# Kernel tuning notes

Measured on AMD Instinct MI355X. Metric: run time of the kernel, lower is better.

## Reference

```python
import jax, jax.numpy as jnp
import numpy as np

D_MODEL = 1024
NHEAD = 16
HEAD_DIM = D_MODEL // NHEAD
DFF = 4096
EPS = 1e-5


def _layernorm(x, g, b):
    mu = jnp.mean(x, axis=-1, keepdims=True)
    var = jnp.mean(jnp.square(x - mu), axis=-1, keepdims=True)
    return (x - mu) * jax.lax.rsqrt(var + EPS) * g + b


def setup_inputs() -> dict:
    key = jax.random.key(0)
    ks = jax.random.split(key, 20)
    B, S = 2, 2048
    s = 0.02
    inp = {
        "src": jax.random.normal(ks[0], (B, S, D_MODEL), jnp.float32),
        "recompute_idx": jnp.sort(jax.random.randint(ks[1], (409,), 0, S)),
        "cached_k": jax.random.normal(ks[2], (B, NHEAD, S, HEAD_DIM), jnp.float32),
        "cached_v": jax.random.normal(ks[3], (B, NHEAD, S, HEAD_DIM), jnp.float32),
        "Wq": jax.random.normal(ks[4], (D_MODEL, D_MODEL), jnp.float32) * s,
        "bq": jnp.zeros((D_MODEL,), jnp.float32),
        "Wk": jax.random.normal(ks[5], (D_MODEL, D_MODEL), jnp.float32) * s,
        "bk": jnp.zeros((D_MODEL,), jnp.float32),
        "Wv": jax.random.normal(ks[6], (D_MODEL, D_MODEL), jnp.float32) * s,
        "bv": jnp.zeros((D_MODEL,), jnp.float32),
        "Wo": jax.random.normal(ks[7], (D_MODEL, D_MODEL), jnp.float32) * s,
        "bo": jnp.zeros((D_MODEL,), jnp.float32),
        "W1": jax.random.normal(ks[8], (DFF, D_MODEL), jnp.float32) * s,
        "b1": jnp.zeros((DFF,), jnp.float32),
        "W2": jax.random.normal(ks[9], (D_MODEL, DFF), jnp.float32) * s,
        "b2": jnp.zeros((D_MODEL,), jnp.float32),
        "g1": jnp.ones((D_MODEL,), jnp.float32),
        "beta1": jnp.zeros((D_MODEL,), jnp.float32),
        "g2": jnp.ones((D_MODEL,), jnp.float32),
        "beta2": jnp.zeros((D_MODEL,), jnp.float32),
    }
    return inp


def reference(src, recompute_idx, cached_k, cached_v, Wq, bq, Wk, bk, Wv, bv,
              Wo, bo, W1, b1, W2, b2, g1, beta1, g2, beta2):
    B, S, D = src.shape
    H, hd = NHEAD, HEAD_DIM

    # Q for all tokens
    q = (src @ Wq.T + bq).reshape(B, S, H, hd).transpose(0, 2, 1, 3)  # [B,H,S,hd]

    # K/V recomputed only for selected tokens, scattered over cached KV
    src_rec = src[:, recompute_idx, :]  # [B,R,D]
    R = src_rec.shape[1]
    k_rec = (src_rec @ Wk.T + bk).reshape(B, R, H, hd).transpose(0, 2, 1, 3)
    v_rec = (src_rec @ Wv.T + bv).reshape(B, R, H, hd).transpose(0, 2, 1, 3)
    k_full = cached_k.at[:, :, recompute_idx, :].set(k_rec)  # [B,H,S,hd]
    v_full = cached_v.at[:, :, recompute_idx, :].set(v_rec)

    # attention over mixed cached/fresh KV
    scores = jnp.einsum('bhqd,bhkd->bhqk', q, k_full) / np.sqrt(hd).astype(src.dtype)
    probs = jax.nn.softmax(scores, axis=-1)
    attn = jnp.einsum('bhqk,bhkd->bhqd', probs, v_full)
    attn = attn.transpose(0, 2, 1, 3).reshape(B, S, D)
    attn = attn @ Wo.T + bo

    x = _layernorm(src + attn, g1, beta1)
    ff = jax.nn.relu(x @ W1.T + b1) @ W2.T + b2
    x = _layernorm(x + ff, g2, beta2)
    return x
```

## Files before the change

### kernel.cpp

```cpp
#include <hip/hip_runtime.h>
#include <hip/hip_bf16.h>

typedef __attribute__((ext_vector_type(4))) float f32x4;
typedef __attribute__((ext_vector_type(8))) short s16x8;
typedef __attribute__((ext_vector_type(4))) short s16x4;
typedef __attribute__((ext_vector_type(2))) short s16x2;

typedef __attribute__((address_space(1))) const unsigned int guint;
typedef __attribute__((address_space(3))) unsigned int luint;

#define D_MODEL 1024
#define NHEAD 16
#define HEAD_DIM 64
#define DFF 4096
#define SEQ 2048
#define BATCH 2

__device__ __forceinline__ float b2f(short s) {
  union { unsigned int u; float f; } v;
  v.u = ((unsigned int)(unsigned short)s) << 16;
  return v.f;
}
__device__ __forceinline__ short f2b(float f) {
  __hip_bfloat16 h = __float2bfloat16(f);
  return *reinterpret_cast<short*>(&h);
}
__device__ __forceinline__ s16x8 cvt8(f32x4 a, f32x4 b) {
  s16x8 r;
  #pragma unroll
  for (int i = 0; i < 4; ++i) { r[i] = f2b(a[i]); r[i + 4] = f2b(b[i]); }
  return r;
}

template<int MODE, bool AF32, bool WF32>
__global__ __launch_bounds__(256, 3)
void gemm_nt(const void* __restrict__ Av, const void* __restrict__ Wv,
             const float* __restrict__ bias, short* __restrict__ out,
             int M, int N, int K,
             const int* __restrict__ idx, int R,
             const float* __restrict__ bias2)
{
  constexpr bool GLDS = (!AF32 && !WF32);

  const float* Af = (const float*)Av;
  const short* Ab = (const short*)Av;
  const float* Wf = (const float*)Wv;
  const short* Wb = (const short*)Wv;

  const int tid  = threadIdx.x;
  const int lane = tid & 63, wave = tid >> 6;
  const int g = lane >> 4, l15 = lane & 15;
  const int wm = (wave & 1) * 64, wn = (wave >> 1) * 64;

  const int z = (MODE == 6 || MODE == 7) ? blockIdx.z : 0;

  const int nwg = gridDim.x * gridDim.y;
  int lid = blockIdx.y * gridDim.x + blockIdx.x;
  if ((nwg & 7) == 0) lid = (lid & 7) * (nwg >> 3) + (lid >> 3);
  const int bn = lid % gridDim.x, bm = lid / gridDim.x;

  f32x4 acc[4][4] = {};

  if constexpr (GLDS) {
    __shared__ short As[2][128][32];
    __shared__ short Bs[2][128][32];

    const short* Wbase = Wb + ((MODE == 7) ? ((size_t)z << 20) : 0);
    const int kOff = (MODE == 6) ? z * 2048 : 0;
    const int Keff = (MODE == 6) ? 2048 : K;

    const int rA0 = wave * 16 + (lane >> 2);
    const int rA1 = rA0 + 64;
    const int c0  = (lane & 3) * 8;

    auto arow = [&](int r) -> long {
      const int gm = bm * 128 + r;
      const int am = gm < M ? gm : M - 1;
      if (MODE == 3 || MODE == 4 || MODE == 7) {
        const int b0 = am / R;
        return (long)(b0 * SEQ + idx[am - b0 * R]);
      }
      return am;
    };
    const long aR0 = arow(rA0), aR1 = arow(rA1);
    const long wR0 = bn * 128 + rA0, wR1 = bn * 128 + rA1;

    const short* gA0 = Ab + aR0 * K + kOff + c0;
    const short* gA1 = Ab + aR1 * K + kOff + c0;
    const short* gB0 = Wbase + wR0 * K + kOff + c0;
    const short* gB1 = Wbase + wR1 * K + kOff + c0;

    auto stage = [&](int buf, int k0) {
      luint* lA0 = (luint*)((short*)As + buf * 4096 + wave * 512);
      luint* lA1 = (luint*)((short*)As + buf * 4096 + (4 + wave) * 512);
      luint* lB0 = (luint*)((short*)Bs + buf * 4096 + wave * 512);
      luint* lB1 = (luint*)((short*)Bs + buf * 4096 + (4 + wave) * 512);
      __builtin_amdgcn_global_load_lds((guint*)(gA0 + k0), lA0, 16, 0, 0);
      __builtin_amdgcn_global_load_lds((guint*)(gA1 + k0), lA1, 16, 0, 0);
      __builtin_amdgcn_global_load_lds((guint*)(gB0 + k0), lB0, 16, 0, 0);
      __builtin_amdgcn_global_load_lds((guint*)(gB1 + k0), lB1, 16, 0, 0);
    };

    stage(0, 0);
    __syncthreads();
    int cur = 0;
    for (int k0 = 0; k0 < Keff; k0 += 32) {
      const int k1 = k0 + 32;
      if (k1 < Keff) stage(cur ^ 1, k1);

      s16x8 af[4], bf4[4];
      #pragma unroll
      for (int mi = 0; mi < 4; ++mi)
        af[mi] = *(const s16x8*)&As[cur][wm + mi * 16 + l15][g * 8];
      #pragma unroll
      for (int ni = 0; ni < 4; ++ni)
        bf4[ni] = *(const s16x8*)&Bs[cur][wn + ni * 16 + l15][g * 8];
      #pragma unroll
      for (int mi = 0; mi < 4; ++mi)
        #pragma unroll
        for (int ni = 0; ni < 4; ++ni)
          acc[mi][ni] = __builtin_amdgcn_mfma_f32_16x16x32_bf16(af[mi], bf4[ni], acc[mi][ni], 0, 0, 0);

      __syncthreads();
      cur ^= 1;
    }
  } else {
    __shared__ short As[128][40];
    __shared__ short Bs[128][40];
    const int r0 = tid >> 1, c0 = (tid & 1) * 16;
    const int gm0 = bm * 128 + r0;
    const int am0 = gm0 < M ? gm0 : M - 1;
    long aRow0;
    if (MODE == 3 || MODE == 4) {
      const int b0 = am0 / R;
      aRow0 = (long)(b0 * SEQ + idx[am0 - b0 * R]);
    } else {
      aRow0 = am0;
    }
    const long wRow0 = bn * 128 + r0;

    for (int k0 = 0; k0 < K; k0 += 32) {
      __syncthreads();
      if (AF32) {
        f32x4 a0 = *(const f32x4*)(Af + aRow0 * K + k0 + c0);
        f32x4 a1 = *(const f32x4*)(Af + aRow0 * K + k0 + c0 + 4);
        f32x4 a2 = *(const f32x4*)(Af + aRow0 * K + k0 + c0 + 8);
        f32x4 a3 = *(const f32x4*)(Af + aRow0 * K + k0 + c0 + 12);
        *(s16x8*)&As[r0][c0]     = cvt8(a0, a1);
        *(s16x8*)&As[r0][c0 + 8] = cvt8(a2, a3);
      } else {
        *(s16x8*)&As[r0][c0]     = *(const s16x8*)(Ab + aRow0 * K + k0 + c0);
        *(s16x8*)&As[r0][c0 + 8] = *(const s16x8*)(Ab + aRow0 * K + k0 + c0 + 8);
      }
      if (WF32) {
        f32x4 w0 = *(const f32x4*)(Wf + wRow0 * K + k0 + c0);
        f32x4 w1 = *(const f32x4*)(Wf + wRow0 * K + k0 + c0 + 4);
        f32x4 w2 = *(const f32x4*)(Wf + wRow0 * K + k0 + c0 + 8);
        f32x4 w3 = *(const f32x4*)(Wf + wRow0 * K + k0 + c0 + 12);
        *(s16x8*)&Bs[r0][c0]     = cvt8(w0, w1);
        *(s16x8*)&Bs[r0][c0 + 8] = cvt8(w2, w3);
      } else {
        *(s16x8*)&Bs[r0][c0]     = *(const s16x8*)(Wb + wRow0 * K + k0 + c0);
        *(s16x8*)&Bs[r0][c0 + 8] = *(const s16x8*)(Wb + wRow0 * K + k0 + c0 + 8);
      }
      __syncthreads();

      s16x8 af[4], bf4[4];
      #pragma unroll
      for (int mi = 0; mi < 4; ++mi)
        af[mi] = *(const s16x8*)&As[wm + mi * 16 + l15][g * 8];
      #pragma unroll
      for (int ni = 0; ni < 4; ++ni)
        bf4[ni] = *(const s16x8*)&Bs[wn + ni * 16 + l15][g * 8];
      #pragma unroll
      for (int mi = 0; mi < 4; ++mi)
        #pragma unroll
        for (int ni = 0; ni < 4; ++ni)
          acc[mi][ni] = __builtin_amdgcn_mfma_f32_16x16x32_bf16(af[mi], bf4[ni], acc[mi][ni], 0, 0, 0);
    }
  }

  #pragma unroll
  for (int mi = 0; mi < 4; ++mi) {
    #pragma unroll
    for (int ni = 0; ni < 4; ++ni) {
      const int gn = bn * 128 + wn + ni * 16 + l15;
      float bv;
      if (MODE == 6)      bv = 0.f;
      else if (MODE == 7) bv = z ? bias2[gn] : bias[gn];
      else                bv = bias[gn];
      #pragma unroll
      for (int r = 0; r < 4; ++r) {
        const int gm = bm * 128 + wm + mi * 16 + g * 4 + r;
        if (gm >= M) continue;
        float v = acc[mi][ni][r] + bv;
        if (MODE == 1) v = v > 0.f ? v : 0.f;
        if (MODE == 2) v *= 0.125f;
        if (MODE == 0 || MODE == 1) {
          out[(long)gm * N + gn] = f2b(v);
        } else if (MODE == 2) {
          const int b = gm >> 11, s = gm & (SEQ - 1);
          const int h = gn >> 6, d = gn & 63;
          out[(((long)(b * NHEAD + h)) * SEQ + s) * 64 + d] = f2b(v);
        } else if (MODE == 3) {
          const int b = gm / R, s = idx[gm - b * R];
          const int h = gn >> 6, d = gn & 63;
          out[(((long)(b * NHEAD + h)) * SEQ + s) * 64 + d] = f2b(v);
        } else if (MODE == 4) {
          const int b = gm / R, s = idx[gm - b * R];
          const int h = gn >> 6, d = gn & 63;
          out[(((long)(b * NHEAD + h)) * 64 + d) * SEQ + s] = f2b(v);
        } else if (MODE == 6) {
          out[((long)z << 22) + (long)gm * N + gn] = f2b(v);
        } else {
          const int b = gm / R, s = idx[gm - b * R];
          const int h = gn >> 6, d = gn & 63;
          if (z == 0)
            out[(((long)(b * NHEAD + h)) * SEQ + s) * 64 + d] = f2b(v);
          else
            (out + (1L << 22))[(((long)(b * NHEAD + h)) * 64 + d) * SEQ + s] = f2b(v);
        }
      }
    }
  }
}

__global__ __launch_bounds__(256, 2)
void attn_fwd(const short* __restrict__ Q, const short* __restrict__ Kf,
              const short* __restrict__ Vt, short* __restrict__ out)
{
  __shared__ short Kl[2][64][64];
  __shared__ short Vl[2][64][64];

  const int tid  = threadIdx.x;
  const int lane = tid & 63, w = tid >> 6;
  const int g = lane >> 4, l15 = lane & 15;
  const int bh = blockIdx.x;
  const int qt = blockIdx.y;
  const int b  = bh >> 4, h = bh & 15;

  const long base = (long)bh * SEQ * 64;
  const int  q0   = qt * 128 + w * 32;

  s16x8 qf[2][2];
  #pragma unroll
  for (int mi = 0; mi < 2; ++mi)
    #pragma unroll
    for (int c = 0; c < 2; ++c)
      qf[mi][c] = *(const s16x8*)(Q + base + (long)(q0 + mi * 16 + l15) * 64 + c * 32 + g * 8);

  float lsum[2] = {0.f, 0.f};
  f32x4 o[2][4] = {};

  auto ldsw = [](short (*buf)[64], int row, int slot) -> short* {
    return (short*)((char*)&buf[0][0] + row * 128 + ((slot ^ (row & 7)) << 4));
  };

  const int c20 = tid, c21 = tid + 256;
  const int r0 = c20 >> 3, s0 = c20 & 7;
  const int r1 = c21 >> 3, s1 = c21 & 7;

  s16x8 kr[2], vr[2];
  kr[0] = *(const s16x8*)(Kf + base + (long)r0 * 64 + s0 * 8);
  kr[1] = *(const s16x8*)(Kf + base + (long)r1 * 64 + s1 * 8);
  vr[0] = *(const s16x8*)(Vt + base + (long)r0 * SEQ + s0 * 8);
  vr[1] = *(const s16x8*)(Vt + base + (long)r1 * SEQ + s1 * 8);
  *(s16x8*)ldsw(Kl[0], r0, s0) = kr[0];
  *(s16x8*)ldsw(Kl[0], r1, s1) = kr[1];
  *(s16x8*)ldsw(Vl[0], r0, s0) = vr[0];
  *(s16x8*)ldsw(Vl[0], r1, s1) = vr[1];

  int cur = 0;
  for (int t = 0; t < SEQ / 64; ++t) {
    __syncthreads();
    const int kvn = (t + 1) * 64;
    if (kvn < SEQ) {
      kr[0] = *(const s16x8*)(Kf + base + (long)(kvn + r0) * 64 + s0 * 8);
      kr[1] = *(const s16x8*)(Kf + base + (long)(kvn + r1) * 64 + s1 * 8);
      vr[0] = *(const s16x8*)(Vt + base + (long)r0 * SEQ + kvn + s0 * 8);
      vr[1] = *(const s16x8*)(Vt + base + (long)r1 * SEQ + kvn + s1 * 8);
    }

    f32x4 sc[2][4] = {};
    __builtin_amdgcn_s_setprio(1);
    #pragma unroll
    for (int c = 0; c < 2; ++c)
      #pragma unroll
      for (int n = 0; n < 4; ++n) {
        s16x8 kb = *(const s16x8*)ldsw(Kl[cur], n * 16 + l15, c * 4 + g);
        sc[0][n] = __builtin_amdgcn_mfma_f32_16x16x32_bf16(kb, qf[0][c], sc[0][n], 0, 0, 0);
        sc[1][n] = __builtin_amdgcn_mfma_f32_16x16x32_bf16(kb, qf[1][c], sc[1][n], 0, 0, 0);
      }
    __builtin_amdgcn_s_setprio(0);

    s16x8 pa[2][2];
    #pragma unroll
    for (int mi = 0; mi < 2; ++mi) {
      #pragma unroll
      for (int n = 0; n < 4; ++n)
        #pragma unroll
        for (int r = 0; r < 4; ++r) {
          sc[mi][n][r] = __expf(sc[mi][n][r]);
          lsum[mi] += sc[mi][n][r];
        }
      unsigned int wpk[4][2];
      #pragma unroll
      for (int n = 0; n < 4; ++n)
        #pragma unroll
        for (int p = 0; p < 2; ++p)
          asm("v_cvt_pk_bf16_f32 %0, %1, %2"
              : "=v"(wpk[n][p]) : "v"(sc[mi][n][2 * p]), "v"(sc[mi][n][2 * p + 1]));
      #pragma unroll
      for (int c = 0; c < 2; ++c) {
        union { s16x8 v; unsigned int u[4]; } pu;
        #pragma unroll
        for (int p = 0; p < 2; ++p) {
          unsigned int a = wpk[2 * c][p], bb = wpk[2 * c + 1][p];
          asm volatile("v_permlane32_swap_b32 %0, %1" : "+v"(a), "+v"(bb));
          asm volatile("v_permlane16_swap_b32 %0, %1" : "+v"(a), "+v"(bb));
          pu.u[p]     = a;
          pu.u[2 + p] = bb;
        }
        pa[mi][c] = pu.v;
      }
    }

    __builtin_amdgcn_s_setprio(1);
    #pragma unroll
    for (int dt = 0; dt < 4; ++dt)
      #pragma unroll
      for (int c = 0; c < 2; ++c) {
        s16x8 vb = *(const s16x8*)ldsw(Vl[cur], dt * 16 + l15, c * 4 + g);
        o[0][dt] = __builtin_amdgcn_mfma_f32_16x16x32_bf16(pa[0][c], vb, o[0][dt], 0, 0, 0);
        o[1][dt] = __builtin_amdgcn_mfma_f32_16x16x32_bf16(pa[1][c], vb, o[1][dt], 0, 0, 0);
      }
    __builtin_amdgcn_s_setprio(0);

    if (kvn < SEQ) {
      *(s16x8*)ldsw(Kl[cur ^ 1], r0, s0) = kr[0];
      *(s16x8*)ldsw(Kl[cur ^ 1], r1, s1) = kr[1];
      *(s16x8*)ldsw(Vl[cur ^ 1], r0, s0) = vr[0];
      *(s16x8*)ldsw(Vl[cur ^ 1], r1, s1) = vr[1];
    }
    cur ^= 1;
  }

  float inv[2][4];
  #pragma unroll
  for (int mi = 0; mi < 2; ++mi) {
    float tt = lsum[mi];
    tt += __shfl_xor(tt, 16, 64);
    tt += __shfl_xor(tt, 32, 64);
    #pragma unroll
    for (int r = 0; r < 4; ++r)
      inv[mi][r] = 1.0f / __shfl(tt, g * 4 + r, 64);
  }

  #pragma unroll
  for (int mi = 0; mi < 2; ++mi)
    #pragma unroll
    for (int dt = 0; dt < 4; ++dt)
      #pragma unroll
      for (int r = 0; r < 4; ++r) {
        const int q   = q0 + mi * 16 + g * 4 + r;
        const int col = h * 64 + dt * 16 + l15;
        out[((long)(b * SEQ + q)) * D_MODEL + col] = f2b(o[mi][dt][r] * inv[mi][r]);
      }
}

template<bool RES_F32, bool OUT_F32>
__global__ __launch_bounds__(256, 4)
void ln_res(const short* __restrict__ a, const void* __restrict__ resv,
            const float* __restrict__ g, const float* __restrict__ beta,
            void* __restrict__ outv)
{
  __shared__ float red[8];
  const int row = blockIdx.x;
  const int tid = threadIdx.x;
  const int lane = tid & 63, w = tid >> 6;

  s16x4 va = *(const s16x4*)(a + (long)row * D_MODEL + tid * 4);
  float x[4];
  if (RES_F32) {
    f32x4 vr = *(const f32x4*)((const float*)resv + (long)row * D_MODEL + tid * 4);
    #pragma unroll
    for (int i = 0; i < 4; ++i) x[i] = b2f(va[i]) + vr[i];
  } else {
    s16x4 vr = *(const s16x4*)((const short*)resv + (long)row * D_MODEL + tid * 4);
    #pragma unroll
    for (int i = 0; i < 4; ++i) x[i] = b2f(va[i]) + b2f(vr[i]);
  }
  float sum = x[0] + x[1] + x[2] + x[3];
  #pragma unroll
  for (int msk = 32; msk >= 1; msk >>= 1) sum += __shfl_xor(sum, msk, 64);
  if (lane == 0) red[w] = sum;
  __syncthreads();
  sum = red[0] + red[1] + red[2] + red[3];
  const float mu = sum * (1.f / D_MODEL);

  float sq = 0.f;
  #pragma unroll
  for (int i = 0; i < 4; ++i) { float d = x[i] - mu; sq += d * d; }
  #pragma unroll
  for (int msk = 32; msk >= 1; msk >>= 1) sq += __shfl_xor(sq, msk, 64);
  if (lane == 0) red[4 + w] = sq;
  __syncthreads();
  sq = red[4] + red[5] + red[6] + red[7];
  const float rs = rsqrtf(sq * (1.f / D_MODEL) + 1e-5f);

  if (OUT_F32) {
    f32x4 ov;
    #pragma unroll
    for (int i = 0; i < 4; ++i) {
      const int c = tid * 4 + i;
      ov[i] = (x[i] - mu) * rs * g[c] + beta[c];
    }
    *(f32x4*)((float*)outv + (long)row * D_MODEL + tid * 4) = ov;
  } else {
    s16x4 ov;
    #pragma unroll
    for (int i = 0; i < 4; ++i) {
      const int c = tid * 4 + i;
      ov[i] = f2b((x[i] - mu) * rs * g[c] + beta[c]);
    }
    *(s16x4*)((short*)outv + (long)row * D_MODEL + tid * 4) = ov;
  }
}

__global__ __launch_bounds__(256, 4)
void ln_res_ff(const short* __restrict__ p0, const short* __restrict__ p1,
               const float* __restrict__ b2, const short* __restrict__ xres,
               const float* __restrict__ g, const float* __restrict__ beta,
               float* __restrict__ outv)
{
  __shared__ float red[8];
  const int row = blockIdx.x;
  const int tid = threadIdx.x;
  const int lane = tid & 63, w = tid >> 6;

  s16x4 v0 = *(const s16x4*)(p0 + (long)row * D_MODEL + tid * 4);
  s16x4 v1 = *(const s16x4*)(p1 + (long)row * D_MODEL + tid * 4);
  s16x4 vx = *(const s16x4*)(xres + (long)row * D_MODEL + tid * 4);
  f32x4 vb = *(const f32x4*)(b2 + tid * 4);
  float x[4];
  #pragma unroll
  for (int i = 0; i < 4; ++i)
    x[i] = b2f(vx[i]) + b2f(v0[i]) + b2f(v1[i]) + vb[i];

  float sum = x[0] + x[1] + x[2] + x[3];
  #pragma unroll
  for (int msk = 32; msk >= 1; msk >>= 1) sum += __shfl_xor(sum, msk, 64);
  if (lane == 0) red[w] = sum;
  __syncthreads();
  sum = red[0] + red[1] + red[2] + red[3];
  const float mu = sum * (1.f / D_MODEL);

  float sq = 0.f;
  #pragma unroll
  for (int i = 0; i < 4; ++i) { float d = x[i] - mu; sq += d * d; }
  #pragma unroll
  for (int msk = 32; msk >= 1; msk >>= 1) sq += __shfl_xor(sq, msk, 64);
  if (lane == 0) red[4 + w] = sq;
  __syncthreads();
  sq = red[4] + red[5] + red[6] + red[7];
  const float rs = rsqrtf(sq * (1.f / D_MODEL) + 1e-5f);

  f32x4 ov;
  #pragma unroll
  for (int i = 0; i < 4; ++i) {
    const int c = tid * 4 + i;
    ov[i] = (x[i] - mu) * rs * g[c] + beta[c];
  }
  *(f32x4*)(outv + (long)row * D_MODEL + tid * 4) = ov;
}

__global__ void cvt_all(const float* __restrict__ ck, const float* __restrict__ src,
                        const float* __restrict__ Wq, const float* __restrict__ Wk,
                        const float* __restrict__ Wv, const float* __restrict__ Wo,
                        const float* __restrict__ W1, const float* __restrict__ W2,
                        short* __restrict__ k_ws, short* __restrict__ srcb,
                        short* __restrict__ Wqb, short* __restrict__ W1b,
                        short* __restrict__ W2b)
{
  for (int i = blockIdx.x * blockDim.x + threadIdx.x; i < 5242880;
       i += gridDim.x * blockDim.x) {
    const float* s; short* d; int li;
    if      (i < 1048576) { s = ck;  d = k_ws;           li = i; }
    else if (i < 2097152) { s = src; d = srcb;           li = i - 1048576; }
    else if (i < 2359296) { s = Wq;  d = Wqb;            li = i - 2097152; }
    else if (i < 2621440) { s = Wk;  d = Wqb + 1048576;  li = i - 2359296; }
    else if (i < 2883584) { s = Wv;  d = Wqb + 2097152;  li = i - 2621440; }
    else if (i < 3145728) { s = Wo;  d = Wqb + 3145728;  li = i - 2883584; }
    else if (i < 4194304) { s = W1;  d = W1b;            li = i - 3145728; }
    else                  { s = W2;  d = W2b;            li = i - 4194304; }
    f32x4 v = *(const f32x4*)(s + (long)li * 4);
    s16x4 r;
    #pragma unroll
    for (int j = 0; j < 4; ++j) r[j] = f2b(v[j]);
    *(s16x4*)(d + (long)li * 4) = r;
  }
}

__global__ void cvt_v_t(const float* __restrict__ in, short* __restrict__ out)
{
  const int c2 = blockIdx.x * blockDim.x + threadIdx.x;
  const int bh = c2 >> 14;
  const int rem = c2 & 16383;
  const int d = rem & 63;
  const int s0 = (rem >> 6) << 3;
  s16x8 r;
  #pragma unroll
  for (int j = 0; j < 8; ++j)
    r[j] = f2b(in[((long)bh * SEQ + s0 + j) * 64 + d]);
  *(s16x8*)(out + ((long)bh * 64 + d) * SEQ + s0) = r;
}

__global__ void cvt_f32_bf16(const f32x4* __restrict__ in, s16x4* __restrict__ out, int n4)
{
  for (int i = blockIdx.x * blockDim.x + threadIdx.x; i < n4; i += gridDim.x * blockDim.x) {
    f32x4 v = in[i];
    s16x4 r;
    #pragma unroll
    for (int j = 0; j < 4; ++j) r[j] = f2b(v[j]);
    out[i] = r;
  }
}

extern "C" void kernel_launch(void* const* d_in, const int* in_sizes, int n_in,
                              void* d_out, int out_size, void* d_ws, size_t ws_size,
                              hipStream_t stream)
{
  const float* src = (const float*)d_in[0];
  const int*   idx = (const int*)  d_in[1];
  const float* ck  = (const float*)d_in[2];
  const float* cv  = (const float*)d_in[3];
  const float* Wq  = (const float*)d_in[4];
  const float* bq  = (const float*)d_in[5];
  const float* Wk  = (const float*)d_in[6];
  const float* bk  = (const float*)d_in[7];
  const float* Wv  = (const float*)d_in[8];
  const float* bv  = (const float*)d_in[9];
  const float* Wo  = (const float*)d_in[10];
  const float* bo  = (const float*)d_in[11];
  const float* W1  = (const float*)d_in[12];
  const float* b1  = (const float*)d_in[13];
  const float* W2  = (const float*)d_in[14];
  const float* b2  = (const float*)d_in[15];
  const float* g1  = (const float*)d_in[16];
  const float* be1 = (const float*)d_in[17];
  const float* g2  = (const float*)d_in[18];
  const float* be2 = (const float*)d_in[19];
  float* out = (float*)d_out;

  char* ws = (char*)d_ws;
  const size_t SZ = (size_t)4096 * 1024 * 2;
  short* x_ws    = (short*)(ws);
  short* proj_ws = (short*)(ws + SZ);
  short* q_ws    = (short*)(ws + 2 * SZ);
  short* k_ws    = (short*)(ws + 3 * SZ);
  short* v_ws    = (short*)(ws + 4 * SZ);
  short* attn_ws = (short*)(ws + 5 * SZ);
  short* h_ws    = (short*)(ws + 2 * SZ);
  short* ff_ws   = proj_ws;
  short* W1b     = (short*)(ws + 6 * SZ);
  short* W2b     = (short*)(ws + 7 * SZ);
  short* srcb    = (short*)(ws + 8 * SZ);
  short* Wqb     = (short*)(ws + 9 * SZ);
  short* Wkb     = Wqb + 1048576;
  const bool big = ws_size >= 10 * SZ;

  const int M = BATCH * SEQ;
  const int R = 409;
  const int Mr = BATCH * R;
  const int nkv4 = BATCH * NHEAD * SEQ * HEAD_DIM / 4;

  cvt_v_t<<<2048, 256, 0, stream>>>(cv, v_ws);

  if (big) {
    cvt_all<<<2048, 256, 0, stream>>>(ck, src, Wq, Wk, Wv, Wo, W1, W2,
                                      k_ws, srcb, Wqb, W1b, W2b);

    gemm_nt<2, false, false><<<dim3(8, 32), 256, 0, stream>>>(srcb, Wqb, bq, q_ws, M, 1024, 1024, nullptr, 0, nullptr);
    gemm_nt<7, false, false><<<dim3(8, 7, 2), 256, 0, stream>>>(srcb, Wkb, bk, k_ws, Mr, 1024, 1024, idx, R, bv);
    attn_fwd<<<dim3(BATCH * NHEAD, SEQ / 128), 256, 0, stream>>>(q_ws, k_ws, v_ws, attn_ws);
    gemm_nt<0, false, false><<<dim3(8, 32), 256, 0, stream>>>(attn_ws, Wqb + 3145728, bo, proj_ws, M, 1024, 1024, nullptr, 0, nullptr);
    ln_res<true, false><<<4096, 256, 0, stream>>>(proj_ws, src, g1, be1, x_ws);
    gemm_nt<1, false, false><<<dim3(32, 32), 256, 0, stream>>>(x_ws, W1b, b1, h_ws, M, DFF, 1024, nullptr, 0, nullptr);
    gemm_nt<6, false, false><<<dim3(8, 32, 2), 256, 0, stream>>>(h_ws, W2b, nullptr, srcb, M, 1024, 4096, nullptr, 0, nullptr);
    ln_res_ff<<<4096, 256, 0, stream>>>(srcb, Wqb, b2, x_ws, g2, be2, out);
  } else {
    cvt_f32_bf16<<<2048, 256, 0, stream>>>((const f32x4*)ck, (s16x4*)k_ws, nkv4);
    gemm_nt<2, true, true><<<dim3(8, 32), 256, 0, stream>>>(src, Wq, bq, q_ws, M, 1024, 1024, nullptr, 0, nullptr);
    gemm_nt<3, true, true><<<dim3(8, 7), 256, 0, stream>>>(src, Wk, bk, k_ws, Mr, 1024, 1024, idx, R, nullptr);
    gemm_nt<4, true, true><<<dim3(8, 7), 256, 0, stream>>>(src, Wv, bv, v_ws, Mr, 1024, 1024, idx, R, nullptr);
    attn_fwd<<<dim3(BATCH * NHEAD, SEQ / 128), 256, 0, stream>>>(q_ws, k_ws, v_ws, attn_ws);
    gemm_nt<0, false, true><<<dim3(8, 32), 256, 0, stream>>>(attn_ws, Wo, bo, proj_ws, M, 1024, 1024, nullptr, 0, nullptr);
    ln_res<true, false><<<4096, 256, 0, stream>>>(proj_ws, src, g1, be1, x_ws);
    gemm_nt<1, false, true><<<dim3(32, 32), 256, 0, stream>>>(x_ws, W1, b1, h_ws, M, DFF, 1024, nullptr, 0, nullptr);
    gemm_nt<0, false, true><<<dim3(8, 32), 256, 0, stream>>>(h_ws, W2, b2, ff_ws, M, 1024, DFF, nullptr, 0, nullptr);
    ln_res<false, true><<<4096, 256, 0, stream>>>(ff_ws, x_ws, g2, be2, out);
  }
}
```

Baseline: 275.7 us.

## Merge Q/K/V projections into one launch and split-K the out-proj and FFN2 GEMMs

Folds the V-cache transpose into the bulk conversion kernel and merges the Q projection with the gathered K and V projections into a single grid. The attention output projection is split into 2 K-slices and the second FFN GEMM into 4, with the partial sums added inside the layernorm kernels. The aim is to cut launch count, raise parallelism, and fill more CUs on small GEMMs. In exchange the layernorms read more bf16 partial buffers, and the merged conversion kernel does a strided V transpose.

```diff
diff --git a/kernel.cpp b/kernel.cpp
--- a/kernel.cpp
+++ b/kernel.cpp
@@ -38,7 +38,9 @@
              const float* __restrict__ bias, short* __restrict__ out,
              int M, int N, int K,
              const int* __restrict__ idx, int R,
-             const float* __restrict__ bias2)
+             const float* __restrict__ bias2, const float* __restrict__ bias3,
+             short* __restrict__ pB, short* __restrict__ pC,
+             short* __restrict__ pD)
 {
   constexpr bool GLDS = (!AF32 && !WF32);
 
@@ -52,12 +54,18 @@
   const int g = lane >> 4, l15 = lane & 15;
   const int wm = (wave & 1) * 64, wn = (wave >> 1) * 64;
 
-  const int z = (MODE == 6 || MODE == 7) ? blockIdx.z : 0;
-
   const int nwg = gridDim.x * gridDim.y;
   int lid = blockIdx.y * gridDim.x + blockIdx.x;
   if ((nwg & 7) == 0) lid = (lid & 7) * (nwg >> 3) + (lid >> 3);
-  const int bn = lid % gridDim.x, bm = lid / gridDim.x;
+  const int bn = lid % gridDim.x;
+  const int bm0 = lid / gridDim.x;
+
+  int task = 0, bm = bm0, Mt = M;
+  if (MODE == 8) {
+    if (bm0 < 32)      { task = 0; bm = bm0;      Mt = M; }
+    else if (bm0 < 39) { task = 1; bm = bm0 - 32; Mt = BATCH * R; }
+    else               { task = 2; bm = bm0 - 39; Mt = BATCH * R; }
+  }
 
   f32x4 acc[4][4] = {};
 
@@ -65,9 +73,10 @@
     __shared__ short As[2][128][32];
     __shared__ short Bs[2][128][32];
 
-    const short* Wbase = Wb + ((MODE == 7) ? ((size_t)z << 20) : 0);
-    const int kOff = (MODE == 6) ? z * 2048 : 0;
-    const int Keff = (MODE == 6) ? 2048 : K;
+    const short* Wbase = Wb + ((MODE == 8) ? ((size_t)task << 20) : 0);
+    const int nz   = (MODE == 6) ? gridDim.z : 1;
+    const int Keff = K / nz;
+    const int kOff = (MODE == 6) ? (int)blockIdx.z * Keff : 0;
 
     const int rA0 = wave * 16 + (lane >> 2);
     const int rA1 = rA0 + 64;
@@ -75,8 +84,8 @@
 
     auto arow = [&](int r) -> long {
       const int gm = bm * 128 + r;
-      const int am = gm < M ? gm : M - 1;
-      if (MODE == 3 || MODE == 4 || MODE == 7) {
+      const int am = gm < Mt ? gm : Mt - 1;
+      if (MODE == 8 && task > 0) {
         const int b0 = am / R;
         return (long)(b0 * SEQ + idx[am - b0 * R]);
       }
@@ -180,6 +189,12 @@
     }
   }
 
+  short* outz = out;
+  if (MODE == 6) {
+    const int z = blockIdx.z;
+    outz = (z == 0) ? out : (z == 1) ? pB : (z == 2) ? pC : pD;
+  }
+
   #pragma unroll
   for (int mi = 0; mi < 4; ++mi) {
     #pragma unroll
@@ -187,12 +202,13 @@
       const int gn = bn * 128 + wn + ni * 16 + l15;
       float bv;
       if (MODE == 6)      bv = 0.f;
-      else if (MODE == 7) bv = z ? bias2[gn] : bias[gn];
+      else if (MODE == 8) bv = (task == 0) ? bias[gn] : (task == 1) ? bias2[gn] : bias3[gn];
       else                bv = bias[gn];
       #pragma unroll
       for (int r = 0; r < 4; ++r) {
         const int gm = bm * 128 + wm + mi * 16 + g * 4 + r;
-        if (gm >= M) continue;
+        if (MODE == 8) { if (gm >= Mt) continue; }
+        else           { if (gm >= M)  continue; }
         float v = acc[mi][ni][r] + bv;
         if (MODE == 1) v = v > 0.f ? v : 0.f;
         if (MODE == 2) v *= 0.125f;
@@ -211,14 +227,19 @@
           const int h = gn >> 6, d = gn & 63;
           out[(((long)(b * NHEAD + h)) * 64 + d) * SEQ + s] = f2b(v);
         } else if (MODE == 6) {
-          out[((long)z << 22) + (long)gm * N + gn] = f2b(v);
+          outz[(long)gm * N + gn] = f2b(v);
         } else {
-          const int b = gm / R, s = idx[gm - b * R];
           const int h = gn >> 6, d = gn & 63;
-          if (z == 0)
-            out[(((long)(b * NHEAD + h)) * SEQ + s) * 64 + d] = f2b(v);
-          else
-            (out + (1L << 22))[(((long)(b * NHEAD + h)) * 64 + d) * SEQ + s] = f2b(v);
+          if (task == 0) {
+            const int b = gm >> 11, s = gm & (SEQ - 1);
+            out[(((long)(b * NHEAD + h)) * SEQ + s) * 64 + d] = f2b(v * 0.125f);
+          } else if (task == 1) {
+            const int b = gm / R, s = idx[gm - b * R];
+            (out + (1L << 22))[(((long)(b * NHEAD + h)) * SEQ + s) * 64 + d] = f2b(v);
+          } else {
+            const int b = gm / R, s = idx[gm - b * R];
+            (out + (1L << 23))[(((long)(b * NHEAD + h)) * 64 + d) * SEQ + s] = f2b(v);
+          }
         }
       }
     }
@@ -370,7 +391,8 @@
 
 template<bool RES_F32, bool OUT_F32>
 __global__ __launch_bounds__(256, 4)
-void ln_res(const short* __restrict__ a, const void* __restrict__ resv,
+void ln_ff2(const short* __restrict__ p0, const short* __restrict__ p1,
+            const float* __restrict__ bias, const void* __restrict__ resv,
             const float* __restrict__ g, const float* __restrict__ beta,
             void* __restrict__ outv)
 {
@@ -379,17 +401,20 @@
   const int tid = threadIdx.x;
   const int lane = tid & 63, w = tid >> 6;
 
-  s16x4 va = *(const s16x4*)(a + (long)row * D_MODEL + tid * 4);
+  s16x4 v0 = *(const s16x4*)(p0 + (long)row * D_MODEL + tid * 4);
+  s16x4 v1 = *(const s16x4*)(p1 + (long)row * D_MODEL + tid * 4);
+  f32x4 vb = *(const f32x4*)(bias + tid * 4);
   float x[4];
   if (RES_F32) {
     f32x4 vr = *(const f32x4*)((const float*)resv + (long)row * D_MODEL + tid * 4);
     #pragma unroll
-    for (int i = 0; i < 4; ++i) x[i] = b2f(va[i]) + vr[i];
+    for (int i = 0; i < 4; ++i) x[i] = vr[i] + b2f(v0[i]) + b2f(v1[i]) + vb[i];
   } else {
     s16x4 vr = *(const s16x4*)((const short*)resv + (long)row * D_MODEL + tid * 4);
     #pragma unroll
-    for (int i = 0; i < 4; ++i) x[i] = b2f(va[i]) + b2f(vr[i]);
-  }
+    for (int i = 0; i < 4; ++i) x[i] = b2f(vr[i]) + b2f(v0[i]) + b2f(v1[i]) + vb[i];
+  }
+
   float sum = x[0] + x[1] + x[2] + x[3];
   #pragma unroll
   for (int msk = 32; msk >= 1; msk >>= 1) sum += __shfl_xor(sum, msk, 64);
@@ -428,10 +453,11 @@
 }
 
 __global__ __launch_bounds__(256, 4)
-void ln_res_ff(const short* __restrict__ p0, const short* __restrict__ p1,
-               const float* __restrict__ b2, const short* __restrict__ xres,
-               const float* __restrict__ g, const float* __restrict__ beta,
-               float* __restrict__ outv)
+void ln_ff4(const short* __restrict__ p0, const short* __restrict__ p1,
+            const short* __restrict__ p2, const short* __restrict__ p3,
+            const float* __restrict__ bias, const short* __restrict__ xres,
+            const float* __restrict__ g, const float* __restrict__ beta,
+            float* __restrict__ outv)
 {
   __shared__ float red[8];
   const int row = blockIdx.x;
@@ -440,12 +466,14 @@
 
   s16x4 v0 = *(const s16x4*)(p0 + (long)row * D_MODEL + tid * 4);
   s16x4 v1 = *(const s16x4*)(p1 + (long)row * D_MODEL + tid * 4);
+  s16x4 v2 = *(const s16x4*)(p2 + (long)row * D_MODEL + tid * 4);
+  s16x4 v3 = *(const s16x4*)(p3 + (long)row * D_MODEL + tid * 4);
   s16x4 vx = *(const s16x4*)(xres + (long)row * D_MODEL + tid * 4);
-  f32x4 vb = *(const f32x4*)(b2 + tid * 4);
+  f32x4 vb = *(const f32x4*)(bias + tid * 4);
   float x[4];
   #pragma unroll
   for (int i = 0; i < 4; ++i)
-    x[i] = b2f(vx[i]) + b2f(v0[i]) + b2f(v1[i]) + vb[i];
+    x[i] = b2f(vx[i]) + b2f(v0[i]) + b2f(v1[i]) + b2f(v2[i]) + b2f(v3[i]) + vb[i];
 
   float sum = x[0] + x[1] + x[2] + x[3];
   #pragma unroll
@@ -474,16 +502,90 @@
   *(f32x4*)(outv + (long)row * D_MODEL + tid * 4) = ov;
 }
 
-__global__ void cvt_all(const float* __restrict__ ck, const float* __restrict__ src,
+template<bool RES_F32, bool OUT_F32>
+__global__ __launch_bounds__(256, 4)
+void ln_res(const short* __restrict__ a, const void* __restrict__ resv,
+            const float* __restrict__ g, const float* __restrict__ beta,
+            void* __restrict__ outv)
+{
+  __shared__ float red[8];
+  const int row = blockIdx.x;
+  const int tid = threadIdx.x;
+  const int lane = tid & 63, w = tid >> 6;
+
+  s16x4 va = *(const s16x4*)(a + (long)row * D_MODEL + tid * 4);
+  float x[4];
+  if (RES_F32) {
+    f32x4 vr = *(const f32x4*)((const float*)resv + (long)row * D_MODEL + tid * 4);
+    #pragma unroll
+    for (int i = 0; i < 4; ++i) x[i] = b2f(va[i]) + vr[i];
+  } else {
+    s16x4 vr = *(const s16x4*)((const short*)resv + (long)row * D_MODEL + tid * 4);
+    #pragma unroll
+    for (int i = 0; i < 4; ++i) x[i] = b2f(va[i]) + b2f(vr[i]);
+  }
+  float sum = x[0] + x[1] + x[2] + x[3];
+  #pragma unroll
+  for (int msk = 32; msk >= 1; msk >>= 1) sum += __shfl_xor(sum, msk, 64);
+  if (lane == 0) red[w] = sum;
+  __syncthreads();
+  sum = red[0] + red[1] + red[2] + red[3];
+  const float mu = sum * (1.f / D_MODEL);
+
+  float sq = 0.f;
+  #pragma unroll
+  for (int i = 0; i < 4; ++i) { float d = x[i] - mu; sq += d * d; }
+  #pragma unroll
+  for (int msk = 32; msk >= 1; msk >>= 1) sq += __shfl_xor(sq, msk, 64);
+  if (lane == 0) red[4 + w] = sq;
+  __syncthreads();
+  sq = red[4] + red[5] + red[6] + red[7];
+  const float rs = rsqrtf(sq * (1.f / D_MODEL) + 1e-5f);
+
+  if (OUT_F32) {
+    f32x4 ov;
+    #pragma unroll
+    for (int i = 0; i < 4; ++i) {
+      const int c = tid * 4 + i;
+      ov[i] = (x[i] - mu) * rs * g[c] + beta[c];
+    }
+    *(f32x4*)((float*)outv + (long)row * D_MODEL + tid * 4) = ov;
+  } else {
+    s16x4 ov;
+    #pragma unroll
+    for (int i = 0; i < 4; ++i) {
+      const int c = tid * 4 + i;
+      ov[i] = f2b((x[i] - mu) * rs * g[c] + beta[c]);
+    }
+    *(s16x4*)((short*)outv + (long)row * D_MODEL + tid * 4) = ov;
+  }
+}
+
+__global__ void cvt_all(const float* __restrict__ ck, const float* __restrict__ cv,
+                        const float* __restrict__ src,
                         const float* __restrict__ Wq, const float* __restrict__ Wk,
                         const float* __restrict__ Wv, const float* __restrict__ Wo,
                         const float* __restrict__ W1, const float* __restrict__ W2,
-                        short* __restrict__ k_ws, short* __restrict__ srcb,
+                        short* __restrict__ k_ws, short* __restrict__ v_ws,
+                        short* __restrict__ srcb,
                         short* __restrict__ Wqb, short* __restrict__ W1b,
                         short* __restrict__ W2b)
 {
-  for (int i = blockIdx.x * blockDim.x + threadIdx.x; i < 5242880;
+  for (int i = blockIdx.x * blockDim.x + threadIdx.x; i < 5767168;
        i += gridDim.x * blockDim.x) {
+    if (i >= 5242880) {
+      const int j = i - 5242880;
+      const int bh = j >> 14;
+      const int rem = j & 16383;
+      const int d = rem & 63;
+      const int s0 = (rem >> 6) << 3;
+      s16x8 r;
+      #pragma unroll
+      for (int k = 0; k < 8; ++k)
+        r[k] = f2b(cv[((long)bh * SEQ + s0 + k) * 64 + d]);
+      *(s16x8*)(v_ws + ((long)bh * 64 + d) * SEQ + s0) = r;
+      continue;
+    }
     const float* s; short* d; int li;
     if      (i < 1048576) { s = ck;  d = k_ws;           li = i; }
     else if (i < 2097152) { s = src; d = srcb;           li = i - 1048576; }
@@ -561,12 +663,10 @@
   short* v_ws    = (short*)(ws + 4 * SZ);
   short* attn_ws = (short*)(ws + 5 * SZ);
   short* h_ws    = (short*)(ws + 2 * SZ);
-  short* ff_ws   = proj_ws;
   short* W1b     = (short*)(ws + 6 * SZ);
   short* W2b     = (short*)(ws + 7 * SZ);
   short* srcb    = (short*)(ws + 8 * SZ);
   short* Wqb     = (short*)(ws + 9 * SZ);
-  short* Wkb     = Wqb + 1048576;
   const bool big = ws_size >= 10 * SZ;
 
   const int M = BATCH * SEQ;
@@ -574,30 +674,40 @@
   const int Mr = BATCH * R;
   const int nkv4 = BATCH * NHEAD * SEQ * HEAD_DIM / 4;
 
-  cvt_v_t<<<2048, 256, 0, stream>>>(cv, v_ws);
-
   if (big) {
-    cvt_all<<<2048, 256, 0, stream>>>(ck, src, Wq, Wk, Wv, Wo, W1, W2,
-                                      k_ws, srcb, Wqb, W1b, W2b);
-
-    gemm_nt<2, false, false><<<dim3(8, 32), 256, 0, stream>>>(srcb, Wqb, bq, q_ws, M, 1024, 1024, nullptr, 0, nullptr);
-    gemm_nt<7, false, false><<<dim3(8, 7, 2), 256, 0, stream>>>(srcb, Wkb, bk, k_ws, Mr, 1024, 1024, idx, R, bv);
+    cvt_all<<<2048, 256, 0, stream>>>(ck, cv, src, Wq, Wk, Wv, Wo, W1, W2,
+                                      k_ws, v_ws, srcb, Wqb, W1b, W2b);
+    gemm_nt<8, false, false><<<dim3(8, 46), 256, 0, stream>>>(
+        srcb, Wqb, bq, q_ws, M, 1024, 1024, idx, R, bk, bv, nullptr, nullptr, nullptr);
     attn_fwd<<<dim3(BATCH * NHEAD, SEQ / 128), 256, 0, stream>>>(q_ws, k_ws, v_ws, attn_ws);
-    gemm_nt<0, false, false><<<dim3(8, 32), 256, 0, stream>>>(attn_ws, Wqb + 3145728, bo, proj_ws, M, 1024, 1024, nullptr, 0, nullptr);
-    ln_res<true, false><<<4096, 256, 0, stream>>>(proj_ws, src, g1, be1, x_ws);
-    gemm_nt<1, false, false><<<dim3(32, 32), 256, 0, stream>>>(x_ws, W1b, b1, h_ws, M, DFF, 1024, nullptr, 0, nullptr);
-    gemm_nt<6, false, false><<<dim3(8, 32, 2), 256, 0, stream>>>(h_ws, W2b, nullptr, srcb, M, 1024, 4096, nullptr, 0, nullptr);
-    ln_res_ff<<<4096, 256, 0, stream>>>(srcb, Wqb, b2, x_ws, g2, be2, out);
+    gemm_nt<6, false, false><<<dim3(8, 32, 2), 256, 0, stream>>>(
+        attn_ws, Wqb + 3145728, nullptr, proj_ws, M, 1024, 1024, nullptr, 0,
+        nullptr, nullptr, q_ws, nullptr, nullptr);
+    ln_ff2<true, false><<<4096, 256, 0, stream>>>(proj_ws, q_ws, bo, src, g1, be1, x_ws);
+    gemm_nt<1, false, false><<<dim3(32, 32), 256, 0, stream>>>(
+        x_ws, W1b, b1, h_ws, M, DFF, 1024, nullptr, 0, nullptr, nullptr,
+        nullptr, nullptr, nullptr);
+    gemm_nt<6, false, false><<<dim3(8, 32, 4), 256, 0, stream>>>(
+        h_ws, W2b, nullptr, proj_ws, M, 1024, 4096, nullptr, 0,
+        nullptr, nullptr, W1b, srcb, Wqb);
+    ln_ff4<<<4096, 256, 0, stream>>>(proj_ws, W1b, srcb, Wqb, b2, x_ws, g2, be2, out);
   } else {
     cvt_f32_bf16<<<2048, 256, 0, stream>>>((const f32x4*)ck, (s16x4*)k_ws, nkv4);
-    gemm_nt<2, true, true><<<dim3(8, 32), 256, 0, stream>>>(src, Wq, bq, q_ws, M, 1024, 1024, nullptr, 0, nullptr);
-    gemm_nt<3, true, true><<<dim3(8, 7), 256, 0, stream>>>(src, Wk, bk, k_ws, Mr, 1024, 1024, idx, R, nullptr);
-    gemm_nt<4, true, true><<<dim3(8, 7), 256, 0, stream>>>(src, Wv, bv, v_ws, Mr, 1024, 1024, idx, R, nullptr);
+    cvt_v_t<<<2048, 256, 0, stream>>>(cv, v_ws);
+    gemm_nt<2, true, true><<<dim3(8, 32), 256, 0, stream>>>(
+        src, Wq, bq, q_ws, M, 1024, 1024, nullptr, 0, nullptr, nullptr, nullptr, nullptr, nullptr);
+    gemm_nt<3, true, true><<<dim3(8, 7), 256, 0, stream>>>(
+        src, Wk, bk, k_ws, Mr, 1024, 1024, idx, R, nullptr, nullptr, nullptr, nullptr, nullptr);
+    gemm_nt<4, true, true><<<dim3(8, 7), 256, 0, stream>>>(
+        src, Wv, bv, v_ws, Mr, 1024, 1024, idx, R, nullptr, nullptr, nullptr, nullptr, nullptr);
     attn_fwd<<<dim3(BATCH * NHEAD, SEQ / 128), 256, 0, stream>>>(q_ws, k_ws, v_ws, attn_ws);
-    gemm_nt<0, false, true><<<dim3(8, 32), 256, 0, stream>>>(attn_ws, Wo, bo, proj_ws, M, 1024, 1024, nullptr, 0, nullptr);
+    gemm_nt<0, false, true><<<dim3(8, 32), 256, 0, stream>>>(
+        attn_ws, Wo, bo, proj_ws, M, 1024, 1024, nullptr, 0, nullptr, nullptr, nullptr, nullptr, nullptr);
     ln_res<true, false><<<4096, 256, 0, stream>>>(proj_ws, src, g1, be1, x_ws);
-    gemm_nt<1, false, true><<<dim3(32, 32), 256, 0, stream>>>(x_ws, W1, b1, h_ws, M, DFF, 1024, nullptr, 0, nullptr);
-    gemm_nt<0, false, true><<<dim3(8, 32), 256, 0, stream>>>(h_ws, W2, b2, ff_ws, M, 1024, DFF, nullptr, 0, nullptr);
-    ln_res<false, true><<<4096, 256, 0, stream>>>(ff_ws, x_ws, g2, be2, out);
-  }
-}
+    gemm_nt<1, false, true><<<dim3(32, 32), 256, 0, stream>>>(
+        x_ws, W1, b1, h_ws, M, DFF, 1024, nullptr, 0, nullptr, nullptr, nullptr, nullptr, nullptr);
+    gemm_nt<0, false, true><<<dim3(8, 32), 256, 0, stream>>>(
+        h_ws, W2, b2, proj_ws, M, 1024, DFF, nullptr, 0, nullptr, nullptr, nullptr, nullptr, nullptr);
+    ln_res<false, true><<<4096, 256, 0, stream>>>(proj_ws, x_ws, g2, be2, out);
+  }
+}
```

Result: faster. 255.8 us (-7.2%).
